# Optimization experiments

Measured on AMD Instinct MI355X. Metric: run time of the kernel, lower is better.

The kernel has to match this reference:

```python
import jax, jax.numpy as jnp
import numpy as np

N_HEADS = 16
D_EMBED = 1024
D_HEAD = D_EMBED // N_HEADS
CAUSAL = False


def setup_inputs() -> dict:
    key = jax.random.key(0)
    k1, k2, k3, k4, k5 = jax.random.split(key, 5)
    B, S, D = 4, 2048, D_EMBED
    scale = 1.0 / np.sqrt(D)
    return {
        "x": jax.random.normal(k1, (B, S, D), dtype=jnp.float32),
        "w_in": jax.random.normal(k2, (D, 3 * D), dtype=jnp.float32) * scale,
        "b_in": jax.random.normal(k3, (3 * D,), dtype=jnp.float32) * 0.02,
        "w_out": jax.random.normal(k4, (D, D), dtype=jnp.float32) * scale,
        "b_out": jax.random.normal(k5, (D,), dtype=jnp.float32) * 0.02,
    }


def reference(x, w_in, b_in, w_out, b_out):
    B, S, D = x.shape
    qkv = jnp.einsum("bsd,de->bse", x, w_in) + b_in  # [B,S,3D]
    q, k, v = jnp.split(qkv, 3, axis=-1)
    # split heads -> [B,H,S,Dh]
    def sh(t):
        return t.reshape(B, S, N_HEADS, D_HEAD).transpose(0, 2, 1, 3)
    q, k, v = sh(q), sh(k), sh(v)
    weight = jnp.einsum("bhsd,bhtd->bhst", q, k)  # [B,H,S,S]
    if CAUSAL:
        mask = jnp.triu(jnp.ones((S, S), dtype=bool), k=1)
        weight = jnp.where(mask, -jnp.inf, weight)
    weight = weight / np.sqrt(D_HEAD)
    weight = jax.nn.softmax(weight, axis=-1)
    out = jnp.einsum("bhst,bhtd->bhsd", weight, v)
    out = out.transpose(0, 2, 1, 3).reshape(B, S, D)
    return jnp.einsum("bsd,de->bse", out, w_out) + b_out
```

## Files before the change

kernel.cpp:

```cpp
#include <hip/hip_runtime.h>
#include <hip/hip_bf16.h>

typedef unsigned short u16;
typedef __attribute__((ext_vector_type(8))) short bf16x8;
typedef __attribute__((ext_vector_type(4))) float f32x4;
typedef __attribute__((ext_vector_type(16))) float f32x16;

#define QSCALE 0.180336880f

#define DEV static __device__ __forceinline__

DEV u16 f2bf(float f) {
  union { float f; unsigned u; } v; v.f = f;
  unsigned r = v.u + 0x7fffu + ((v.u >> 16) & 1u);
  return (u16)(r >> 16);
}

DEV unsigned pk2(float a, float b) {
  union { __hip_bfloat162 h; unsigned u; } c;
  c.h = __float22bfloat162_rn(make_float2(a, b));
  return c.u;
}

DEV void gll16(void* lds, const void* g) {
  __builtin_amdgcn_global_load_lds(
      (const __attribute__((address_space(1))) unsigned int*)g,
      (__attribute__((address_space(3))) unsigned int*)lds, 16, 0, 0);
}

DEV void transpose_tile(const float* __restrict__ W, u16* __restrict__ Wt,
                        int K, int N, int k0, int n0, float scl, int tid,
                        u16 (*t)[65]) {
  const int rr = tid >> 4;
  const int cc = (tid & 15) * 4;
#pragma unroll
  for (int i = 0; i < 4; ++i) {
    const int row = rr * 4 + i;
    float4 f = *(const float4*)&W[(size_t)(k0 + row) * N + n0 + cc];
    t[row][cc + 0] = f2bf(f.x * scl);
    t[row][cc + 1] = f2bf(f.y * scl);
    t[row][cc + 2] = f2bf(f.z * scl);
    t[row][cc + 3] = f2bf(f.w * scl);
  }
  __syncthreads();
#pragma unroll
  for (int i = 0; i < 4; ++i) {
    const int n = rr * 4 + i;
    ushort4 u;
    u.x = t[cc + 0][n]; u.y = t[cc + 1][n]; u.z = t[cc + 2][n]; u.w = t[cc + 3][n];
    *(ushort4*)&Wt[(size_t)(n0 + n) * K + k0 + cc] = u;
  }
}

__global__ __launch_bounds__(256) void pack_all(const float* __restrict__ x,
                                                const float* __restrict__ w_in,
                                                const float* __restrict__ w_out,
                                                u16* __restrict__ Xbf,
                                                u16* __restrict__ WinT,
                                                u16* __restrict__ WoutT) {
  __shared__ u16 t[64][65];
  const int bid = blockIdx.x;
  const int tid = threadIdx.x;
  if (bid < 2048) {
    const int n4 = 8192 * 1024 / 4;
    for (int i = bid * 256 + tid; i < n4; i += 2048 * 256) {
      float4 f = ((const float4*)x)[i];
      ushort4 u;
      u.x = f2bf(f.x); u.y = f2bf(f.y); u.z = f2bf(f.z); u.w = f2bf(f.w);
      ((ushort4*)Xbf)[i] = u;
    }
  } else if (bid < 2048 + 768) {
    const int tb = bid - 2048;
    const int k0 = (tb & 15) * 64, n0 = (tb >> 4) * 64;
    const float scl = (n0 < 1024) ? QSCALE : 1.0f;
    transpose_tile(w_in, WinT, 1024, 3072, k0, n0, scl, tid, t);
  } else {
    const int tb = bid - 2816;
    const int k0 = (tb & 15) * 64, n0 = (tb >> 4) * 64;
    transpose_tile(w_out, WoutT, 1024, 1024, k0, n0, 1.0f, tid, t);
  }
}

__global__ __launch_bounds__(256) void transpose_v(const u16* __restrict__ qkv,
                                                   u16* __restrict__ vT) {
  __shared__ u16 t[64][72];
  const int bh = blockIdx.y;
  const int b = bh >> 4, h = bh & 15;
  const int t0 = blockIdx.x * 64;
  const int tid = threadIdx.x;
  const int row = tid >> 2;
  const int cg = (tid & 3) * 16;
  const size_t src = (size_t)b * 2048 * 3072 + (size_t)(t0 + row) * 3072 + 2048 + h * 64 + cg;
  bf16x8 v0 = *(const bf16x8*)&qkv[src];
  bf16x8 v1 = *(const bf16x8*)&qkv[src + 8];
#pragma unroll
  for (int i = 0; i < 8; ++i) { t[row][cg + i] = (u16)v0[i]; t[row][cg + 8 + i] = (u16)v1[i]; }
  __syncthreads();
  const int d = tid >> 2;
  const int tg = (tid & 3) * 16;
  bf16x8 o0, o1;
#pragma unroll
  for (int i = 0; i < 8; ++i) { o0[i] = (short)t[tg + i][d]; o1[i] = (short)t[tg + 8 + i][d]; }
  u16* dst = &vT[((size_t)bh * 64 + d) * 2048 + t0 + tg];
  *(bf16x8*)dst = o0;
  *(bf16x8*)(dst + 8) = o1;
}


#define G1_STAGE(S)                                                   \
  {                                                                   \
    gll16((u16*)L1[S] + wave * 512, g0); g0 += 32;                    \
    gll16((u16*)L1[S] + 4096 + wave * 512, g1); g1 += 32;             \
    gll16((u16*)L1[S] + 8192 + wave * 512, g2); g2 += 32;             \
    gll16((u16*)L1[S] + 12288 + wave * 512, g3); g3 += 32;            \
  }

#define G1_BODY(S, ISSUE, VM)                                         \
  {                                                                   \
    if (ISSUE) G1_STAGE((S + 2) & 3)                                  \
    asm volatile("s_waitcnt vmcnt(" #VM ")" ::: "memory");            \
    __builtin_amdgcn_s_barrier();                                     \
    const char* sb = (const char*)L1[S];                              \
    bf16x8 af[8], bfr[4];                                             \
    _Pragma("unroll")                                                 \
    for (int m = 0; m < 8; ++m) af[m] = *(const bf16x8*)(sb + aoff[m]); \
    _Pragma("unroll")                                                 \
    for (int n = 0; n < 4; ++n) bfr[n] = *(const bf16x8*)(sb + boff[n]); \
    __builtin_amdgcn_s_setprio(1);                                    \
    _Pragma("unroll")                                                 \
    for (int m = 0; m < 8; ++m)                                       \
      _Pragma("unroll")                                               \
      for (int n = 0; n < 4; ++n)                                     \
        acc[m][n] = __builtin_amdgcn_mfma_f32_16x16x32_bf16(af[m], bfr[n], acc[m][n], 0, 0, 0); \
    __builtin_amdgcn_s_setprio(0);                                    \
  }

__global__ __launch_bounds__(512, 2) void gemm1_256(const u16* __restrict__ A,
                                                    const u16* __restrict__ Bt,
                                                    const float* __restrict__ bias,
                                                    u16* __restrict__ C) {
  __shared__ __align__(16) u16 L1[4][16384];
  const int tid = threadIdx.x;
  const int wave = tid >> 6, lane = tid & 63;
  const int g = lane >> 4, lr = lane & 15;
  const int wr = wave >> 2, wc = wave & 3;
  const int id = blockIdx.x;
  const int xcd = id & 7, j = id >> 3;
  const int bm = (xcd * 4 + (j & 3)) * 256;
  const int bn = (j >> 2) * 256;

  int aoff[8], boff[4];
#pragma unroll
  for (int m = 0; m < 8; ++m)
    aoff[m] = wr * 8192 + m * 1024 + g * 256 + lr * 16;
#pragma unroll
  for (int n = 0; n < 4; ++n)
    boff[n] = 16384 + wc * 4096 + n * 1024 + g * 256 + lr * 16;

  const u16* g0; const u16* g1; const u16* g2; const u16* g3;
  {
    const int b0 = wave * 1024 + lane * 16;
    const int plane = b0 >> 8, lrr = (b0 >> 4) & 15, pb = b0 & 15;
    const int row = (plane >> 2) * 16 + lrr;
    const int kc = (plane & 3) * 8 + (pb >> 1);
    g0 = A  + (size_t)(bm + row) * 1024 + kc;
    g1 = A  + (size_t)(bm + 128 + row) * 1024 + kc;
    g2 = Bt + (size_t)(bn + row) * 1024 + kc;
    g3 = Bt + (size_t)(bn + 128 + row) * 1024 + kc;
  }

  f32x4 acc[8][4] = {};

  G1_STAGE(0)
  G1_STAGE(1)

  for (int it = 0; it < 7; ++it) {
    G1_BODY(0, 1, 8) G1_BODY(1, 1, 8) G1_BODY(2, 1, 8) G1_BODY(3, 1, 8)
  }
  G1_BODY(0, 1, 8)
  G1_BODY(1, 1, 8)
  G1_BODY(2, 0, 4)
  G1_BODY(3, 0, 0)

#pragma unroll
  for (int m = 0; m < 8; ++m) {
#pragma unroll
    for (int n = 0; n < 4; ++n) {
      const int col = bn + wc * 64 + n * 16 + lr;
      float bv = bias[col];
      if (col < 1024) bv *= QSCALE;
#pragma unroll
      for (int r = 0; r < 4; ++r) {
        const int row = bm + wr * 128 + m * 16 + g * 4 + r;
        C[(size_t)row * 3072 + col] = f2bf(acc[m][n][r] + bv);
      }
    }
  }
}

template<bool OUT_BF16>
__global__ __launch_bounds__(256) void gemm_bf16(const u16* __restrict__ A,
                                                 const u16* __restrict__ Bt,
                                                 const float* __restrict__ bias,
                                                 void* __restrict__ Cout,
                                                 int M, int N, int K, int qn) {
  __shared__ __align__(16) u16 As[128][64];
  __shared__ __align__(16) u16 Bs[128][64];
  const int tid = threadIdx.x;
  const int wave = tid >> 6, lane = tid & 63;
  const int g = lane >> 4, lr = lane & 15;
  const int lid = blockIdx.y * gridDim.x + blockIdx.x;
  const int chunk = gridDim.x >> 3;
  const int xcd = lid & 7, j = lid >> 3;
  const int bm = (xcd * chunk + (j % chunk)) * 128;
  const int bn = (j / chunk) * 128;
  const int wm = (wave >> 1) * 64, wn = (wave & 1) * 64;
  f32x4 acc[4][4] = {};
  for (int kt = 0; kt < K; kt += 64) {
    __syncthreads();
#pragma unroll
    for (int jj = 0; jj < 4; ++jj) {
      int chnk = wave * 4 + jj;
      int e = chnk * 512 + lane * 8;
      int r = e >> 6, c = e & 63;
      gll16((u16*)As + chnk * 512, &A[(size_t)(bm + r) * K + kt + c]);
      gll16((u16*)Bs + chnk * 512, &Bt[(size_t)(bn + r) * K + kt + c]);
    }
    __syncthreads();
#pragma unroll
    for (int kk = 0; kk < 64; kk += 32) {
      bf16x8 af[4], bfr[4];
#pragma unroll
      for (int m = 0; m < 4; ++m)
        af[m] = *(const bf16x8*)&As[wm + m * 16 + lr][kk + g * 8];
#pragma unroll
      for (int n = 0; n < 4; ++n)
        bfr[n] = *(const bf16x8*)&Bs[wn + n * 16 + lr][kk + g * 8];
#pragma unroll
      for (int m = 0; m < 4; ++m)
#pragma unroll
        for (int n = 0; n < 4; ++n)
          acc[m][n] = __builtin_amdgcn_mfma_f32_16x16x32_bf16(af[m], bfr[n], acc[m][n], 0, 0, 0);
    }
  }
#pragma unroll
  for (int m = 0; m < 4; ++m) {
#pragma unroll
    for (int n = 0; n < 4; ++n) {
      const int col = bn + wn + n * 16 + lr;
      float bv = bias ? bias[col] : 0.f;
      if (col < qn) bv *= QSCALE;
#pragma unroll
      for (int r = 0; r < 4; ++r) {
        const int row = bm + wm + m * 16 + g * 4 + r;
        float v = acc[m][n][r] + bv;
        if (OUT_BF16) ((u16*)Cout)[(size_t)row * N + col] = f2bf(v);
        else          ((float*)Cout)[(size_t)row * N + col] = v;
      }
    }
  }
}


#define ATTN_BODY(BUF, ISSUE, VM)                                                 \
  {                                                                               \
    if (ISSUE) {                                                                  \
      gll16((u16*)Ks[((BUF) + 2) & 3] + wave * 512, gk); gk += 32 * 3072;         \
      gll16((u16*)Vs[((BUF) + 2) & 3] + wave * 512, gv); gv += 32;                \
    }                                                                             \
    asm volatile("s_waitcnt vmcnt(" #VM ")" ::: "memory");                        \
    __builtin_amdgcn_s_barrier();                                                 \
    const char* kb = (const char*)Ks[(BUF)];                                      \
    const char* vb = (const char*)Vs[(BUF)];                                      \
    f32x16 s = {};                                                                \
    __builtin_amdgcn_s_setprio(1);                                                \
    _Pragma("unroll")                                                             \
    for (int kk = 0; kk < 4; ++kk) {                                              \
      bf16x8 kf = *(const bf16x8*)(kb + koff[kk]);                                \
      s = __builtin_amdgcn_mfma_f32_32x32x16_bf16(kf, qf[kk], s, 0, 0, 0);        \
    }                                                                             \
    __builtin_amdgcn_s_setprio(0);                                                \
    float pr[16];                                                                 \
    _Pragma("unroll")                                                             \
    for (int r = 0; r < 16; ++r) pr[r] = __builtin_amdgcn_exp2f(s[r]);            \
    lsum += ((pr[0] + pr[1]) + (pr[2] + pr[3])) + ((pr[4] + pr[5]) + (pr[6] + pr[7])) \
          + ((pr[8] + pr[9]) + (pr[10] + pr[11])) + ((pr[12] + pr[13]) + (pr[14] + pr[15])); \
    union { unsigned u[4]; bf16x8 v; } pa0, pa1;                                  \
    {                                                                             \
      unsigned X0 = pk2(pr[0], pr[1]), X1 = pk2(pr[2], pr[3]);                    \
      unsigned Y0 = pk2(pr[4], pr[5]), Y1 = pk2(pr[6], pr[7]);                    \
      asm volatile("v_permlane32_swap_b32 %0, %1" : "+v"(X0), "+v"(Y0));          \
      asm volatile("v_permlane32_swap_b32 %0, %1" : "+v"(X1), "+v"(Y1));          \
      pa0.u[0] = X0; pa0.u[1] = X1; pa0.u[2] = Y0; pa0.u[3] = Y1;                 \
      unsigned Z0 = pk2(pr[8], pr[9]), Z1 = pk2(pr[10], pr[11]);                  \
      unsigned W0 = pk2(pr[12], pr[13]), W1 = pk2(pr[14], pr[15]);                \
      asm volatile("v_permlane32_swap_b32 %0, %1" : "+v"(Z0), "+v"(W0));          \
      asm volatile("v_permlane32_swap_b32 %0, %1" : "+v"(Z1), "+v"(W1));          \
      pa1.u[0] = Z0; pa1.u[1] = Z1; pa1.u[2] = W0; pa1.u[3] = W1;                 \
    }                                                                             \
    __builtin_amdgcn_s_setprio(1);                                                \
    {                                                                             \
      bf16x8 vf00 = *(const bf16x8*)(vb + voff[0][0]);                            \
      bf16x8 vf10 = *(const bf16x8*)(vb + voff[1][0]);                            \
      o0 = __builtin_amdgcn_mfma_f32_32x32x16_bf16(pa0.v, vf00, o0, 0, 0, 0);     \
      o1 = __builtin_amdgcn_mfma_f32_32x32x16_bf16(pa0.v, vf10, o1, 0, 0, 0);     \
      bf16x8 vf01 = *(const bf16x8*)(vb + voff[0][1]);                            \
      bf16x8 vf11 = *(const bf16x8*)(vb + voff[1][1]);                            \
      o0 = __builtin_amdgcn_mfma_f32_32x32x16_bf16(pa1.v, vf01, o0, 0, 0, 0);     \
      o1 = __builtin_amdgcn_mfma_f32_32x32x16_bf16(pa1.v, vf11, o1, 0, 0, 0);     \
    }                                                                             \
    __builtin_amdgcn_s_setprio(0);                                                \
  }

__global__ __launch_bounds__(256, 4) void attn_kernel(const u16* __restrict__ qkv,
                                                      const u16* __restrict__ vT,
                                                      u16* __restrict__ out) {
  __shared__ __align__(16) u16 Ks[4][2048];
  __shared__ __align__(16) u16 Vs[4][2048];
  const int tid = threadIdx.x;
  const int wave = tid >> 6, lane = tid & 63;
  const int hi = lane >> 5, l31 = lane & 31;
  const int id = blockIdx.x;
  const int bh = ((id >> 3) & 7) * 8 + (id & 7);
  const int b = bh >> 4, h = bh & 15;
  const int q0 = (id >> 6) * 128;
  const size_t base = (size_t)b * 2048 * 3072;
  const u16* kg = qkv + base + 1024 + h * 64;
  const u16* vg = vT + (size_t)bh * 64 * 2048;

  const int qrow = q0 + wave * 32 + l31;
  bf16x8 qf[4];
#pragma unroll
  for (int kk = 0; kk < 4; ++kk)
    qf[kk] = *(const bf16x8*)&qkv[base + (size_t)qrow * 3072 + h * 64 + kk * 16 + hi * 8];

  int koff[4];
#pragma unroll
  for (int kk = 0; kk < 4; ++kk)
    koff[kk] = (kk * 2 + hi) * 512 + l31 * 16;
  int voff[2][2];
#pragma unroll
  for (int dt = 0; dt < 2; ++dt)
#pragma unroll
    for (int kp = 0; kp < 2; ++kp)
      voff[dt][kp] = (dt * 4 + kp * 2 + hi) * 512 + l31 * 16;

  const u16* gk = kg + (size_t)l31 * 3072 + wave * 16 + hi * 8;
  const u16* gv = vg + (size_t)((wave >> 1) * 32 + l31) * 2048 + (wave & 1) * 16 + hi * 8;

  f32x16 o0 = {}, o1 = {};
  float lsum = 0.f;

  gll16((u16*)Ks[0] + wave * 512, gk); gk += 32 * 3072;
  gll16((u16*)Vs[0] + wave * 512, gv); gv += 32;
  gll16((u16*)Ks[1] + wave * 512, gk); gk += 32 * 3072;
  gll16((u16*)Vs[1] + wave * 512, gv); gv += 32;

  for (int it4 = 0; it4 < 15; ++it4) {
    ATTN_BODY(0, true, 4)
    ATTN_BODY(1, true, 4)
    ATTN_BODY(2, true, 4)
    ATTN_BODY(3, true, 4)
  }
  ATTN_BODY(0, true, 4)
  ATTN_BODY(1, true, 4)
  ATTN_BODY(2, false, 2)
  ATTN_BODY(3, false, 0)

  float lt = lsum + __shfl_xor(lsum, 32);
  const size_t orow0 = (size_t)b * 2048 + q0 + wave * 32;
#pragma unroll
  for (int r = 0; r < 16; ++r) {
    const int crow = (r & 3) + 8 * (r >> 2) + 4 * hi;
    const float li = __shfl(lt, crow);
    u16* orow = out + (orow0 + crow) * 1024 + h * 64 + l31;
    orow[0]  = f2bf(o0[r] / li);
    orow[32] = f2bf(o1[r] / li);
  }
}

extern "C" void kernel_launch(void* const* d_in, const int* in_sizes, int n_in,
                              void* d_out, int out_size, void* d_ws, size_t ws_size,
                              hipStream_t stream) {
  (void)in_sizes; (void)n_in; (void)out_size; (void)ws_size;
  const float* x     = (const float*)d_in[0];
  const float* w_in  = (const float*)d_in[1];
  const float* b_in  = (const float*)d_in[2];
  const float* w_out = (const float*)d_in[3];
  const float* b_out = (const float*)d_in[4];
  float* out = (float*)d_out;

  char* ws = (char*)d_ws;
  u16* Xbf   = (u16*)ws; ws += (size_t)8192 * 1024 * 2;
  u16* WinT  = (u16*)ws; ws += (size_t)3072 * 1024 * 2;
  u16* WoutT = (u16*)ws; ws += (size_t)1024 * 1024 * 2;
  u16* qkv   = (u16*)ws; ws += (size_t)8192 * 3072 * 2;
  u16* attno = (u16*)ws;
  u16* vT    = Xbf;

  pack_all<<<3072, 256, 0, stream>>>(x, w_in, w_out, Xbf, WinT, WoutT);
  gemm1_256<<<384, 512, 0, stream>>>(Xbf, WinT, b_in, qkv);
  transpose_v<<<dim3(32, 64), 256, 0, stream>>>(qkv, vT);
  attn_kernel<<<1024, 256, 0, stream>>>(qkv, vT, attno);
  gemm_bf16<false><<<dim3(64, 8), 256, 0, stream>>>(attno, WoutT, b_out, out, 8192, 1024, 1024, 0);
}
```

Measured before the change: 221.0 us.

## Replace output projection GEMM with 256x128 tile, 4-stage pipelined kernel

Replaces the generic 128x128 single-buffered output-projection GEMM with a specialized 256x128-tile kernel using 512 threads. Global-to-LDS loads go through a 4-slot ring that runs two stages ahead, with explicit vmcnt waits and barriers, and s_setprio raises priority around the MFMA blocks. This targets exposed load latency and the double __syncthreads per k-step of the old kernel. The grid shrinks to 256 blocks with hardcoded dimensions, which may underfill the CUs and ties the kernel to this problem shape.

```diff
diff --git a/kernel.cpp b/kernel.cpp
--- a/kernel.cpp
+++ b/kernel.cpp
@@ -198,64 +198,90 @@
   }
 }
 
-template<bool OUT_BF16>
-__global__ __launch_bounds__(256) void gemm_bf16(const u16* __restrict__ A,
-                                                 const u16* __restrict__ Bt,
-                                                 const float* __restrict__ bias,
-                                                 void* __restrict__ Cout,
-                                                 int M, int N, int K, int qn) {
-  __shared__ __align__(16) u16 As[128][64];
-  __shared__ __align__(16) u16 Bs[128][64];
+
+#define G2_STAGE(S)                                                   \
+  {                                                                   \
+    gll16((u16*)L2[S] + wave * 512, g0); g0 += 32;                    \
+    gll16((u16*)L2[S] + 4096 + wave * 512, g1); g1 += 32;             \
+    gll16((u16*)L2[S] + 8192 + wave * 512, g2); g2 += 32;             \
+  }
+
+#define G2_BODY(S, ISSUE, VM)                                         \
+  {                                                                   \
+    if (ISSUE) G2_STAGE((S + 2) & 3)                                  \
+    asm volatile("s_waitcnt vmcnt(" #VM ")" ::: "memory");            \
+    __builtin_amdgcn_s_barrier();                                     \
+    const char* sb = (const char*)L2[S];                              \
+    bf16x8 af[8], bfr[2];                                             \
+    _Pragma("unroll")                                                 \
+    for (int m = 0; m < 8; ++m) af[m] = *(const bf16x8*)(sb + aoff[m]); \
+    _Pragma("unroll")                                                 \
+    for (int n = 0; n < 2; ++n) bfr[n] = *(const bf16x8*)(sb + boff[n]); \
+    __builtin_amdgcn_s_setprio(1);                                    \
+    _Pragma("unroll")                                                 \
+    for (int m = 0; m < 8; ++m)                                       \
+      _Pragma("unroll")                                               \
+      for (int n = 0; n < 2; ++n)                                     \
+        acc[m][n] = __builtin_amdgcn_mfma_f32_16x16x32_bf16(af[m], bfr[n], acc[m][n], 0, 0, 0); \
+    __builtin_amdgcn_s_setprio(0);                                    \
+  }
+
+__global__ __launch_bounds__(512, 2) void gemm2_256(const u16* __restrict__ A,
+                                                    const u16* __restrict__ Bt,
+                                                    const float* __restrict__ bias,
+                                                    float* __restrict__ C) {
+  __shared__ __align__(16) u16 L2[4][12288];
   const int tid = threadIdx.x;
   const int wave = tid >> 6, lane = tid & 63;
   const int g = lane >> 4, lr = lane & 15;
-  const int lid = blockIdx.y * gridDim.x + blockIdx.x;
-  const int chunk = gridDim.x >> 3;
-  const int xcd = lid & 7, j = lid >> 3;
-  const int bm = (xcd * chunk + (j % chunk)) * 128;
-  const int bn = (j / chunk) * 128;
-  const int wm = (wave >> 1) * 64, wn = (wave & 1) * 64;
-  f32x4 acc[4][4] = {};
-  for (int kt = 0; kt < K; kt += 64) {
-    __syncthreads();
-#pragma unroll
-    for (int jj = 0; jj < 4; ++jj) {
-      int chnk = wave * 4 + jj;
-      int e = chnk * 512 + lane * 8;
-      int r = e >> 6, c = e & 63;
-      gll16((u16*)As + chnk * 512, &A[(size_t)(bm + r) * K + kt + c]);
-      gll16((u16*)Bs + chnk * 512, &Bt[(size_t)(bn + r) * K + kt + c]);
-    }
-    __syncthreads();
-#pragma unroll
-    for (int kk = 0; kk < 64; kk += 32) {
-      bf16x8 af[4], bfr[4];
-#pragma unroll
-      for (int m = 0; m < 4; ++m)
-        af[m] = *(const bf16x8*)&As[wm + m * 16 + lr][kk + g * 8];
-#pragma unroll
-      for (int n = 0; n < 4; ++n)
-        bfr[n] = *(const bf16x8*)&Bs[wn + n * 16 + lr][kk + g * 8];
-#pragma unroll
-      for (int m = 0; m < 4; ++m)
-#pragma unroll
-        for (int n = 0; n < 4; ++n)
-          acc[m][n] = __builtin_amdgcn_mfma_f32_16x16x32_bf16(af[m], bfr[n], acc[m][n], 0, 0, 0);
-    }
-  }
-#pragma unroll
-  for (int m = 0; m < 4; ++m) {
-#pragma unroll
-    for (int n = 0; n < 4; ++n) {
-      const int col = bn + wn + n * 16 + lr;
-      float bv = bias ? bias[col] : 0.f;
-      if (col < qn) bv *= QSCALE;
+  const int wr = wave >> 2, wc = wave & 3;
+  const int id = blockIdx.x;
+  const int xcd = id & 7, j = id >> 3;
+  const int bm = (xcd * 4 + (j & 3)) * 256;
+  const int bn = (j >> 2) * 128;
+
+  int aoff[8], boff[2];
+#pragma unroll
+  for (int m = 0; m < 8; ++m)
+    aoff[m] = wr * 8192 + m * 1024 + g * 256 + lr * 16;
+#pragma unroll
+  for (int n = 0; n < 2; ++n)
+    boff[n] = 16384 + (wc * 2 + n) * 1024 + g * 256 + lr * 16;
+
+  const u16* g0; const u16* g1; const u16* g2;
+  {
+    const int b0 = wave * 1024 + lane * 16;
+    const int plane = b0 >> 8, lrr = (b0 >> 4) & 15, pb = b0 & 15;
+    const int row = (plane >> 2) * 16 + lrr;
+    const int kc = (plane & 3) * 8 + (pb >> 1);
+    g0 = A  + (size_t)(bm + row) * 1024 + kc;
+    g1 = A  + (size_t)(bm + 128 + row) * 1024 + kc;
+    g2 = Bt + (size_t)(bn + row) * 1024 + kc;
+  }
+
+  f32x4 acc[8][2] = {};
+
+  G2_STAGE(0)
+  G2_STAGE(1)
+
+  for (int it = 0; it < 7; ++it) {
+    G2_BODY(0, 1, 6) G2_BODY(1, 1, 6) G2_BODY(2, 1, 6) G2_BODY(3, 1, 6)
+  }
+  G2_BODY(0, 1, 6)
+  G2_BODY(1, 1, 6)
+  G2_BODY(2, 0, 3)
+  G2_BODY(3, 0, 0)
+
+#pragma unroll
+  for (int m = 0; m < 8; ++m) {
+#pragma unroll
+    for (int n = 0; n < 2; ++n) {
+      const int col = bn + wc * 32 + n * 16 + lr;
+      const float bv = bias[col];
 #pragma unroll
       for (int r = 0; r < 4; ++r) {
-        const int row = bm + wm + m * 16 + g * 4 + r;
-        float v = acc[m][n][r] + bv;
-        if (OUT_BF16) ((u16*)Cout)[(size_t)row * N + col] = f2bf(v);
-        else          ((float*)Cout)[(size_t)row * N + col] = v;
+        const int row = bm + wr * 128 + m * 16 + g * 4 + r;
+        C[(size_t)row * 1024 + col] = acc[m][n][r] + bv;
       }
     }
   }
@@ -402,5 +428,5 @@
   gemm1_256<<<384, 512, 0, stream>>>(Xbf, WinT, b_in, qkv);
   transpose_v<<<dim3(32, 64), 256, 0, stream>>>(qkv, vT);
   attn_kernel<<<1024, 256, 0, stream>>>(qkv, vT, attno);
-  gemm_bf16<false><<<dim3(64, 8), 256, 0, stream>>>(attno, WoutT, b_out, out, 8192, 1024, 1024, 0);
-}
+  gemm2_256<<<256, 512, 0, stream>>>(attno, WoutT, b_out, out);
+}
```

New measurement: 218.3 us (median of 2 runs). No clear change (-1.2%).

## Unify both projection GEMMs into a 128x128 four-stage LDS ring kernel

Applied to the files above, without the earlier changes.

Replaces the 256x256 QKV GEMM and the simple double-sync output GEMM with one templated 128x128-tile kernel that uses a 4-deep async global-to-LDS ring with vmcnt waits. The QKV projection now runs 1536 smaller blocks instead of 384 large ones. The output projection gains pipelined loads instead of a sync-load-sync loop. The trade is lower per-block operand reuse and more global traffic for the QKV GEMM, in exchange for more blocks and better latency hiding.

```diff
diff --git a/kernel.cpp b/kernel.cpp
--- a/kernel.cpp
+++ b/kernel.cpp
@@ -107,148 +107,82 @@
 }
 
 
-#define G1_STAGE(S)                                                   \
+#define GG_STAGE(S)                                                   \
   {                                                                   \
-    gll16((u16*)L1[S] + wave * 512, g0); g0 += 32;                    \
-    gll16((u16*)L1[S] + 4096 + wave * 512, g1); g1 += 32;             \
-    gll16((u16*)L1[S] + 8192 + wave * 512, g2); g2 += 32;             \
-    gll16((u16*)L1[S] + 12288 + wave * 512, g3); g3 += 32;            \
-  }
-
-#define G1_BODY(S, ISSUE, VM)                                         \
+    gll16((u16*)Ls[S] + wave * 512, g0); g0 += 32;                    \
+    gll16((u16*)Ls[S] + 2048 + wave * 512, g1); g1 += 32;             \
+    gll16((u16*)Ls[S] + 4096 + wave * 512, g2); g2 += 32;             \
+    gll16((u16*)Ls[S] + 6144 + wave * 512, g3); g3 += 32;             \
+  }
+
+#define GG_BODY(S, ISSUE, VM)                                         \
   {                                                                   \
-    if (ISSUE) G1_STAGE((S + 2) & 3)                                  \
+    if (ISSUE) GG_STAGE((S + 2) & 3)                                  \
     asm volatile("s_waitcnt vmcnt(" #VM ")" ::: "memory");            \
     __builtin_amdgcn_s_barrier();                                     \
-    const char* sb = (const char*)L1[S];                              \
-    bf16x8 af[8], bfr[4];                                             \
+    const char* sb = (const char*)Ls[S];                              \
+    bf16x8 af[4], bfr[4];                                             \
     _Pragma("unroll")                                                 \
-    for (int m = 0; m < 8; ++m) af[m] = *(const bf16x8*)(sb + aoff[m]); \
+    for (int m = 0; m < 4; ++m) af[m] = *(const bf16x8*)(sb + aoff[m]); \
     _Pragma("unroll")                                                 \
     for (int n = 0; n < 4; ++n) bfr[n] = *(const bf16x8*)(sb + boff[n]); \
     __builtin_amdgcn_s_setprio(1);                                    \
     _Pragma("unroll")                                                 \
-    for (int m = 0; m < 8; ++m)                                       \
+    for (int m = 0; m < 4; ++m)                                       \
       _Pragma("unroll")                                               \
       for (int n = 0; n < 4; ++n)                                     \
         acc[m][n] = __builtin_amdgcn_mfma_f32_16x16x32_bf16(af[m], bfr[n], acc[m][n], 0, 0, 0); \
     __builtin_amdgcn_s_setprio(0);                                    \
   }
 
-__global__ __launch_bounds__(512, 2) void gemm1_256(const u16* __restrict__ A,
+template<bool OUT_BF16>
+__global__ __launch_bounds__(256, 2) void gemm_ring(const u16* __restrict__ A,
                                                     const u16* __restrict__ Bt,
                                                     const float* __restrict__ bias,
-                                                    u16* __restrict__ C) {
-  __shared__ __align__(16) u16 L1[4][16384];
+                                                    void* __restrict__ Cout,
+                                                    int N, int qn) {
+  __shared__ __align__(16) u16 Ls[4][8192];
   const int tid = threadIdx.x;
   const int wave = tid >> 6, lane = tid & 63;
   const int g = lane >> 4, lr = lane & 15;
-  const int wr = wave >> 2, wc = wave & 3;
+  const int wm = (wave >> 1) * 64, wn = (wave & 1) * 64;
   const int id = blockIdx.x;
   const int xcd = id & 7, j = id >> 3;
-  const int bm = (xcd * 4 + (j & 3)) * 256;
-  const int bn = (j >> 2) * 256;
-
-  int aoff[8], boff[4];
-#pragma unroll
-  for (int m = 0; m < 8; ++m)
-    aoff[m] = wr * 8192 + m * 1024 + g * 256 + lr * 16;
+  const int bm = (xcd * 8 + (j & 7)) * 128;
+  const int bn = (j >> 3) * 128;
+
+  int aoff[4], boff[4];
+#pragma unroll
+  for (int m = 0; m < 4; ++m)
+    aoff[m] = (((wave >> 1) * 4 + m) * 4 + g) * 256 + lr * 16;
 #pragma unroll
   for (int n = 0; n < 4; ++n)
-    boff[n] = 16384 + wc * 4096 + n * 1024 + g * 256 + lr * 16;
-
-  const u16* g0; const u16* g1; const u16* g2; const u16* g3;
-  {
-    const int b0 = wave * 1024 + lane * 16;
-    const int plane = b0 >> 8, lrr = (b0 >> 4) & 15, pb = b0 & 15;
-    const int row = (plane >> 2) * 16 + lrr;
-    const int kc = (plane & 3) * 8 + (pb >> 1);
-    g0 = A  + (size_t)(bm + row) * 1024 + kc;
-    g1 = A  + (size_t)(bm + 128 + row) * 1024 + kc;
-    g2 = Bt + (size_t)(bn + row) * 1024 + kc;
-    g3 = Bt + (size_t)(bn + 128 + row) * 1024 + kc;
-  }
-
-  f32x4 acc[8][4] = {};
-
-  G1_STAGE(0)
-  G1_STAGE(1)
+    boff[n] = 8192 + (((wave & 1) * 4 + n) * 4 + g) * 256 + lr * 16;
+
+  const u16* g0 = A  + (size_t)(bm + wave * 16 + lr) * 1024 + g * 8;
+  const u16* g1 = g0 + (size_t)64 * 1024;
+  const u16* g2 = Bt + (size_t)(bn + wave * 16 + lr) * 1024 + g * 8;
+  const u16* g3 = g2 + (size_t)64 * 1024;
+
+  f32x4 acc[4][4] = {};
+
+  GG_STAGE(0)
+  GG_STAGE(1)
 
   for (int it = 0; it < 7; ++it) {
-    G1_BODY(0, 1, 8) G1_BODY(1, 1, 8) G1_BODY(2, 1, 8) G1_BODY(3, 1, 8)
-  }
-  G1_BODY(0, 1, 8)
-  G1_BODY(1, 1, 8)
-  G1_BODY(2, 0, 4)
-  G1_BODY(3, 0, 0)
-
-#pragma unroll
-  for (int m = 0; m < 8; ++m) {
-#pragma unroll
-    for (int n = 0; n < 4; ++n) {
-      const int col = bn + wc * 64 + n * 16 + lr;
-      float bv = bias[col];
-      if (col < 1024) bv *= QSCALE;
-#pragma unroll
-      for (int r = 0; r < 4; ++r) {
-        const int row = bm + wr * 128 + m * 16 + g * 4 + r;
-        C[(size_t)row * 3072 + col] = f2bf(acc[m][n][r] + bv);
-      }
-    }
-  }
-}
-
-template<bool OUT_BF16>
-__global__ __launch_bounds__(256) void gemm_bf16(const u16* __restrict__ A,
-                                                 const u16* __restrict__ Bt,
-                                                 const float* __restrict__ bias,
-                                                 void* __restrict__ Cout,
-                                                 int M, int N, int K, int qn) {
-  __shared__ __align__(16) u16 As[128][64];
-  __shared__ __align__(16) u16 Bs[128][64];
-  const int tid = threadIdx.x;
-  const int wave = tid >> 6, lane = tid & 63;
-  const int g = lane >> 4, lr = lane & 15;
-  const int lid = blockIdx.y * gridDim.x + blockIdx.x;
-  const int chunk = gridDim.x >> 3;
-  const int xcd = lid & 7, j = lid >> 3;
-  const int bm = (xcd * chunk + (j % chunk)) * 128;
-  const int bn = (j / chunk) * 128;
-  const int wm = (wave >> 1) * 64, wn = (wave & 1) * 64;
-  f32x4 acc[4][4] = {};
-  for (int kt = 0; kt < K; kt += 64) {
-    __syncthreads();
-#pragma unroll
-    for (int jj = 0; jj < 4; ++jj) {
-      int chnk = wave * 4 + jj;
-      int e = chnk * 512 + lane * 8;
-      int r = e >> 6, c = e & 63;
-      gll16((u16*)As + chnk * 512, &A[(size_t)(bm + r) * K + kt + c]);
-      gll16((u16*)Bs + chnk * 512, &Bt[(size_t)(bn + r) * K + kt + c]);
-    }
-    __syncthreads();
-#pragma unroll
-    for (int kk = 0; kk < 64; kk += 32) {
-      bf16x8 af[4], bfr[4];
-#pragma unroll
-      for (int m = 0; m < 4; ++m)
-        af[m] = *(const bf16x8*)&As[wm + m * 16 + lr][kk + g * 8];
-#pragma unroll
-      for (int n = 0; n < 4; ++n)
-        bfr[n] = *(const bf16x8*)&Bs[wn + n * 16 + lr][kk + g * 8];
-#pragma unroll
-      for (int m = 0; m < 4; ++m)
-#pragma unroll
-        for (int n = 0; n < 4; ++n)
-          acc[m][n] = __builtin_amdgcn_mfma_f32_16x16x32_bf16(af[m], bfr[n], acc[m][n], 0, 0, 0);
-    }
-  }
+    GG_BODY(0, 1, 8) GG_BODY(1, 1, 8) GG_BODY(2, 1, 8) GG_BODY(3, 1, 8)
+  }
+  GG_BODY(0, 1, 8)
+  GG_BODY(1, 1, 8)
+  GG_BODY(2, 0, 4)
+  GG_BODY(3, 0, 0)
+
 #pragma unroll
   for (int m = 0; m < 4; ++m) {
 #pragma unroll
     for (int n = 0; n < 4; ++n) {
       const int col = bn + wn + n * 16 + lr;
-      float bv = bias ? bias[col] : 0.f;
+      float bv = bias[col];
       if (col < qn) bv *= QSCALE;
 #pragma unroll
       for (int r = 0; r < 4; ++r) {
@@ -399,8 +333,8 @@
   u16* vT    = Xbf;
 
   pack_all<<<3072, 256, 0, stream>>>(x, w_in, w_out, Xbf, WinT, WoutT);
-  gemm1_256<<<384, 512, 0, stream>>>(Xbf, WinT, b_in, qkv);
+  gemm_ring<true ><<<1536, 256, 0, stream>>>(Xbf, WinT, b_in, qkv, 3072, 1024);
   transpose_v<<<dim3(32, 64), 256, 0, stream>>>(qkv, vT);
   attn_kernel<<<1024, 256, 0, stream>>>(qkv, vT, attno);
-  gemm_bf16<false><<<dim3(64, 8), 256, 0, stream>>>(attno, WoutT, b_out, out, 8192, 1024, 1024, 0);
-}
+  gemm_ring<false><<<512, 256, 0, stream>>>(attno, WoutT, b_out, out, 1024, 0);
+}
```

Result: slower. 244.9 us (+10.8%).
